# Kernel optimization log

Hardware: AMD Instinct MI355X
Metric: run time of the kernel (lower is better)

The kernel has to match this reference:

```python
import jax, jax.numpy as jnp
import numpy as np

N_NODES = 10000
N_EDGES = 80000
IN_DIM = 768
HID = 256
HEADS = 8
NEG_SLOPE = 0.2


def setup_inputs() -> dict:
    key = jax.random.key(0)
    ks = jax.random.split(key, 12)
    s = 0.02
    x = jax.random.normal(ks[0], (N_NODES, IN_DIM), dtype=jnp.float32)
    edge_index = jax.random.randint(ks[1], (2, N_EDGES), 0, N_NODES, dtype=jnp.int64)
    W1 = jax.random.normal(ks[2], (IN_DIM, HEADS * HID), dtype=jnp.float32) * s
    a_src1 = jax.random.normal(ks[3], (HEADS, HID), dtype=jnp.float32) * s
    a_dst1 = jax.random.normal(ks[4], (HEADS, HID), dtype=jnp.float32) * s
    b1 = jnp.zeros((HEADS * HID,), dtype=jnp.float32)
    W2 = jax.random.normal(ks[5], (HEADS * HID, HEADS * HID), dtype=jnp.float32) * s
    a_src2 = jax.random.normal(ks[6], (HEADS, HID), dtype=jnp.float32) * s
    a_dst2 = jax.random.normal(ks[7], (HEADS, HID), dtype=jnp.float32) * s
    b2 = jnp.zeros((HID,), dtype=jnp.float32)
    # graph_projection: 256 -> 256
    Wp = jax.random.normal(ks[8], (HID, HID), dtype=jnp.float32) * s
    bp = jnp.zeros((HID,), dtype=jnp.float32)
    return dict(x=x, edge_index=edge_index, W1=W1, a_src1=a_src1, a_dst1=a_dst1,
                b1=b1, W2=W2, a_src2=a_src2, a_dst2=a_dst2, b2=b2, Wp=Wp, bp=bp)


def _gat_conv(x, src, dst, W, a_src, a_dst, b, concat):
    """PyG GATConv (eval mode, self-loops already appended to src/dst)."""
    N = x.shape[0]
    H, C = a_src.shape
    h = (x @ W).reshape(N, H, C)                         # [N,H,C] per-head projection
    alpha_s = jnp.sum(h * a_src[None], axis=-1)           # [N,H]
    alpha_d = jnp.sum(h * a_dst[None], axis=-1)           # [N,H]
    e = jax.nn.leaky_relu(alpha_s[src] + alpha_d[dst], NEG_SLOPE)  # [E,H]
    # segment softmax over incoming edges of each dst node
    m = jax.ops.segment_max(e, dst, num_segments=N)       # [N,H]
    m = jnp.where(jnp.isfinite(m), m, 0.0)
    p = jnp.exp(e - m[dst])
    denom = jax.ops.segment_sum(p, dst, num_segments=N)   # [N,H]
    alpha = p / (denom[dst] + 1e-16)                      # [E,H]
    out = jax.ops.segment_sum(alpha[:, :, None] * h[src], dst, num_segments=N)  # [N,H,C]
    if concat:
        return out.reshape(N, H * C) + b
    return out.mean(axis=1) + b


def reference(x, edge_index, W1, a_src1, a_dst1, b1, W2, a_src2, a_dst2, b2, Wp, bp):
    N = x.shape[0]
    loops = jnp.arange(N, dtype=edge_index.dtype)
    src = jnp.concatenate([edge_index[0], loops])
    dst = jnp.concatenate([edge_index[1], loops])
    h = _gat_conv(x, src, dst, W1, a_src1, a_dst1, b1, concat=True)   # [N, 2048]
    h = jax.nn.elu(h)                                                 # dropout: eval/no-op
    h = _gat_conv(h, src, dst, W2, a_src2, a_dst2, b2, concat=False)  # [N, 256]
    h = h @ Wp + bp
    return jax.nn.relu(h)                                             # dropout: eval/no-op
```

## Files before the change

kernel.cpp:

```cpp
#include <hip/hip_runtime.h>
#include <cstdint>
#include <cstddef>

#define IN_DIM  768
#define NNODES  10000
#define MPAD    10240
#define NEDGES  80000
#define E_TOT   90000
#define HEADS   8
#define HID     256
#define HC      2048
#define NEG_SLOPE 0.2f

#define CVT_BLK  ((MPAD * IN_DIM / 4) / 256)
#define CNT_BLK  ((E_TOT + 255) / 256)
#define T1_BLK   ((HC / 32) * (IN_DIM / 32))
#define T2_BLK   ((HC / 32) * (HC / 32))
#define TP_BLK   ((HID / 32) * (HID / 32))
#define PREP_BLK (CVT_BLK + CNT_BLK + T1_BLK + T2_BLK + TP_BLK)

typedef _Float16 __attribute__((ext_vector_type(8))) f16x8;
typedef float    __attribute__((ext_vector_type(4))) f32x4;

__device__ __forceinline__ int edge_src(const int* __restrict__ ei, int e) {
    return (e < NEDGES) ? ei[e] : (e - NEDGES);
}
__device__ __forceinline__ int edge_dst(const int* __restrict__ ei, int e) {
    return (e < NEDGES) ? ei[NEDGES + e] : (e - NEDGES);
}

__device__ __forceinline__ void tcvt_body(
    const float* __restrict__ W, _Float16* __restrict__ T,
    int K, int N, int bx, int by, int t)
{
    __shared__ float tile[32][33];
    int tx = t & 31, ty = t >> 5;
#pragma unroll
    for (int q = 0; q < 4; q++)
        tile[ty + q * 8][tx] = W[(size_t)(by * 32 + ty + q * 8) * N + bx * 32 + tx];
    __syncthreads();
#pragma unroll
    for (int q = 0; q < 4; q++) {
        float v = tile[tx][ty + q * 8];
        T[(size_t)(bx * 32 + ty + q * 8) * K + by * 32 + tx] = (_Float16)v;
    }
}

__global__ __launch_bounds__(256) void prep_kernel(
    const float* __restrict__ x, _Float16* __restrict__ xh,
    const int* __restrict__ ei, int* __restrict__ cnt,
    const float* __restrict__ W1, _Float16* __restrict__ W1t,
    const float* __restrict__ W2, _Float16* __restrict__ W2t,
    const float* __restrict__ Wp, _Float16* __restrict__ Wpt)
{
    int b = blockIdx.x;
    int t = threadIdx.x;
    if (b < CVT_BLK) {
        int i = b * 256 + t;
        size_t e = (size_t)i * 4;
        int r = (int)(e / IN_DIM);
        float4 v = (r < NNODES) ? *(const float4*)(x + e)
                                : make_float4(0.f, 0.f, 0.f, 0.f);
        _Float16 h4[4] = {(_Float16)v.x, (_Float16)v.y, (_Float16)v.z, (_Float16)v.w};
        *(ushort4*)(xh + e) = *(ushort4*)h4;
    } else if (b < CVT_BLK + CNT_BLK) {
        int e = (b - CVT_BLK) * 256 + t;
        if (e < E_TOT) atomicAdd(&cnt[edge_dst(ei, e)], 1);
    } else if (b < CVT_BLK + CNT_BLK + T1_BLK) {
        int idx = b - (CVT_BLK + CNT_BLK);
        tcvt_body(W1, W1t, IN_DIM, HC, idx % (HC / 32), idx / (HC / 32), t);
    } else if (b < CVT_BLK + CNT_BLK + T1_BLK + T2_BLK) {
        int idx = b - (CVT_BLK + CNT_BLK + T1_BLK);
        tcvt_body(W2, W2t, HC, HC, idx % (HC / 32), idx / (HC / 32), t);
    } else {
        int idx = b - (CVT_BLK + CNT_BLK + T1_BLK + T2_BLK);
        tcvt_body(Wp, Wpt, HID, HID, idx % (HID / 32), idx / (HID / 32), t);
    }
}

__global__ void scan_kernel(const int* __restrict__ cnt, int* __restrict__ indptr) {
    __shared__ int sums[1024];
    const int CH = 10;
    int t = threadIdx.x;
    int base = t * CH;
    int s = 0;
#pragma unroll
    for (int i = 0; i < CH; i++) { int idx = base + i; if (idx < NNODES) s += cnt[idx]; }
    sums[t] = s;
    __syncthreads();
    for (int off = 1; off < 1024; off <<= 1) {
        int v = (t >= off) ? sums[t - off] : 0;
        __syncthreads();
        sums[t] += v;
        __syncthreads();
    }
    int run = (t == 0) ? 0 : sums[t - 1];
#pragma unroll
    for (int i = 0; i < CH; i++) {
        int idx = base + i;
        if (idx < NNODES) { indptr[idx] = run; run += cnt[idx]; }
    }
    if (t == 0) indptr[NNODES] = E_TOT;
}

__global__ void scatter_kernel(const int* __restrict__ ei, const int* __restrict__ indptr,
                               int* __restrict__ cur, int* __restrict__ sorted) {
    int e = blockIdx.x * 256 + threadIdx.x;
    if (e < E_TOT) {
        int d = edge_dst(ei, e);
        int pos = atomicAdd(&cur[d], 1);
        sorted[indptr[d] + pos] = e;
    }
}

__global__ __launch_bounds__(512, 2) void gemm8p_kernel(
    const _Float16* __restrict__ A, const _Float16* __restrict__ B,
    _Float16* __restrict__ C, int M, int K, int Nn)
{
    __shared__ __align__(16) _Float16 lds[2][36864];

    const int t = threadIdx.x;
    const int w = t >> 6, lane = t & 63;
    const int fr = lane & 15, q4 = lane >> 4;
    const int wr = w >> 2, wc = w & 3;

    const int nwgx = gridDim.x;
    int wg = blockIdx.y * nwgx + blockIdx.x;
    const int cpx = (nwgx * gridDim.y) >> 3;
    wg = (wg & 7) * cpx + (wg >> 3);
    const int row0 = (wg / nwgx) * 320;
    const int col0 = (wg % nwgx) * 256;

    const int rowt = t >> 3;
    const int scol = ((t & 7) ^ (rowt & 7)) << 3;
    const _Float16* baseA = A + (size_t)(row0 + rowt) * K + scol;
    const _Float16* baseB = B + (size_t)(col0 + rowt) * K + scol;
    const int dstw = w * 512;

    auto stageA = [&](int q, int kel, int bb) {
        __builtin_amdgcn_global_load_lds(
            (const __attribute__((address_space(1))) void*)(baseA + (size_t)q * 64 * K + kel),
            (__attribute__((address_space(3))) void*)&lds[bb][q * 4096 + dstw], 16, 0, 0);
    };
    auto stageB = [&](int q, int kel, int bb) {
        __builtin_amdgcn_global_load_lds(
            (const __attribute__((address_space(1))) void*)(baseB + (size_t)q * 64 * K + kel),
            (__attribute__((address_space(3))) void*)&lds[bb][20480 + q * 4096 + dstw], 16, 0, 0);
    };

    f32x4 acc[2][2][5][2];
#pragma unroll
    for (int qm = 0; qm < 2; qm++)
#pragma unroll
        for (int qn = 0; qn < 2; qn++)
#pragma unroll
            for (int mi = 0; mi < 5; mi++)
#pragma unroll
                for (int ni = 0; ni < 2; ni++)
                    acc[qm][qn][mi][ni] = {0.f, 0.f, 0.f, 0.f};

#define PHASE(QM, QN, BB, STAGE_STMT, WAIT_STMT)                                \
    do {                                                                        \
        f16x8 fa[5][2], fb[2][2];                                               \
        _Pragma("unroll")                                                       \
        for (int mi = 0; mi < 5; mi++) {                                        \
            _Pragma("unroll")                                                   \
            for (int ks = 0; ks < 2; ks++) {                                    \
                int lr = wr * 80 + mi * 16 + fr;                                \
                int sl = ((ks << 2) | q4) ^ (fr & 7);                           \
                fa[mi][ks] = *(const f16x8*)&lds[BB][(QM) * 10240 + (lr << 6) + (sl << 3)]; \
            }                                                                   \
        }                                                                       \
        _Pragma("unroll")                                                       \
        for (int ni = 0; ni < 2; ni++) {                                        \
            _Pragma("unroll")                                                   \
            for (int ks = 0; ks < 2; ks++) {                                    \
                int lr = wc * 32 + ni * 16 + fr;                                \
                int sl = ((ks << 2) | q4) ^ (fr & 7);                           \
                fb[ni][ks] = *(const f16x8*)&lds[BB][20480 + (QN) * 8192 + (lr << 6) + (sl << 3)]; \
            }                                                                   \
        }                                                                       \
        STAGE_STMT;                                                             \
        WAIT_STMT;                                                              \
        __builtin_amdgcn_s_barrier();                                           \
        asm volatile("s_waitcnt lgkmcnt(0)" ::: "memory");                      \
        __builtin_amdgcn_sched_barrier(0);                                      \
        __builtin_amdgcn_s_setprio(1);                                          \
        _Pragma("unroll")                                                       \
        for (int ks = 0; ks < 2; ks++) {                                        \
            _Pragma("unroll")                                                   \
            for (int mi = 0; mi < 5; mi++) {                                    \
                _Pragma("unroll")                                               \
                for (int ni = 0; ni < 2; ni++)                                  \
                    acc[QM][QN][mi][ni] = __builtin_amdgcn_mfma_f32_16x16x32_f16(\
                        fa[mi][ks], fb[ni][ks], acc[QM][QN][mi][ni], 0, 0, 0);  \
            }                                                                   \
        }                                                                       \
        __builtin_amdgcn_s_setprio(0);                                          \
        __builtin_amdgcn_sched_barrier(0);                                      \
        __builtin_amdgcn_s_barrier();                                           \
    } while (0)

#pragma unroll
    for (int q = 0; q < 5; q++) stageA(q, 0, 0);
#pragma unroll
    for (int q = 0; q < 4; q++) stageB(q, 0, 0);
    asm volatile("s_waitcnt vmcnt(0)" ::: "memory");
    __builtin_amdgcn_s_barrier();

    const int nT = K >> 6;
    int t0 = 0;
    for (; t0 < nT - 1; ++t0) {
        int bb = t0 & 1;
        int bn = bb ^ 1;
        int k1 = (t0 + 1) << 6;
        PHASE(0, 0, bb,
              { stageA(0, k1, bn); stageA(1, k1, bn); },
              asm volatile("s_waitcnt vmcnt(6)" ::: "memory"));
        PHASE(1, 0, bb,
              { stageA(2, k1, bn); stageB(0, k1, bn); stageB(1, k1, bn); },
              asm volatile("s_waitcnt vmcnt(7)" ::: "memory"));
        PHASE(0, 1, bb,
              { stageA(3, k1, bn); stageA(4, k1, bn); },
              asm volatile("s_waitcnt vmcnt(7)" ::: "memory"));
        PHASE(1, 1, bb,
              { stageB(2, k1, bn); stageB(3, k1, bn); },
              ((void)0));
    }
    {
        int bb = t0 & 1;
        PHASE(0, 0, bb, ((void)0), asm volatile("s_waitcnt vmcnt(4)" ::: "memory"));
        PHASE(1, 0, bb, ((void)0), asm volatile("s_waitcnt vmcnt(2)" ::: "memory"));
        PHASE(0, 1, bb, ((void)0), asm volatile("s_waitcnt vmcnt(0)" ::: "memory"));
        PHASE(1, 1, bb, ((void)0), ((void)0));
    }
#undef PHASE

#pragma unroll
    for (int qm = 0; qm < 2; qm++)
#pragma unroll
        for (int qn = 0; qn < 2; qn++)
#pragma unroll
            for (int mi = 0; mi < 5; mi++) {
                int mb = row0 + qm * 160 + wr * 80 + mi * 16 + q4 * 4;
#pragma unroll
                for (int ni = 0; ni < 2; ni++) {
                    int n = col0 + qn * 128 + wc * 32 + ni * 16 + fr;
#pragma unroll
                    for (int r = 0; r < 4; r++) {
                        int m = mb + r;
                        if (m < M) C[(size_t)m * Nn + n] = (_Float16)acc[qm][qn][mi][ni][r];
                    }
                }
            }
}

template <int EPI>
__global__ __launch_bounds__(256) void mfma_gemm_kernel(
    const _Float16* __restrict__ A, const _Float16* __restrict__ B,
    void* __restrict__ Cout, const float* __restrict__ bias,
    int M, int K, int Nn, int swz)
{
    __shared__ __align__(16) _Float16 sA[2][128 * 32];
    __shared__ __align__(16) _Float16 sB[2][128 * 32];

    int t = threadIdx.x;
    int bx = blockIdx.x, by = blockIdx.y;
    if (swz) {
        int id = by * 16 + bx;
        int xcd = id & 7, slot = id >> 3;
        bx = 2 * xcd + (slot & 1);
        by = slot >> 1;
    }
    int row0 = by * 128;
    int col0 = bx * 128;

    int s0 = t, s1 = t + 256;
    int m0 = s0 >> 2, k0 = (s0 & 3) * 8;
    int m1 = s1 >> 2, k1 = (s1 & 3) * 8;
    const _Float16* a0 = A + (size_t)(row0 + m0) * K + k0;
    const _Float16* a1 = A + (size_t)(row0 + m1) * K + k1;
    const _Float16* b0 = B + (size_t)(col0 + m0) * K + k0;
    const _Float16* b1 = B + (size_t)(col0 + m1) * K + k1;

    int w = t >> 6, lane = t & 63;
    int wm = (w & 1) * 64, wn = (w >> 1) * 64;
    int fr = lane & 15, quad = lane >> 4;

    auto stage = [&](int kt, int bsel) {
        _Float16* dA0 = &sA[bsel][(w * 64) * 8];
        _Float16* dA1 = &sA[bsel][(w * 64 + 256) * 8];
        _Float16* dB0 = &sB[bsel][(w * 64) * 8];
        _Float16* dB1 = &sB[bsel][(w * 64 + 256) * 8];
        __builtin_amdgcn_global_load_lds(
            (const __attribute__((address_space(1))) void*)(a0 + kt),
            (__attribute__((address_space(3))) void*)dA0, 16, 0, 0);
        __builtin_amdgcn_global_load_lds(
            (const __attribute__((address_space(1))) void*)(a1 + kt),
            (__attribute__((address_space(3))) void*)dA1, 16, 0, 0);
        __builtin_amdgcn_global_load_lds(
            (const __attribute__((address_space(1))) void*)(b0 + kt),
            (__attribute__((address_space(3))) void*)dB0, 16, 0, 0);
        __builtin_amdgcn_global_load_lds(
            (const __attribute__((address_space(1))) void*)(b1 + kt),
            (__attribute__((address_space(3))) void*)dB1, 16, 0, 0);
    };

    f32x4 acc[4][4];
#pragma unroll
    for (int i = 0; i < 4; i++)
#pragma unroll
        for (int j = 0; j < 4; j++) acc[i][j] = {0.f, 0.f, 0.f, 0.f};

    const int nIt = K / 32;
    stage(0, 0);
    __syncthreads();

    for (int it = 0; it < nIt; ++it) {
        int cb = it & 1;
        if (it + 1 < nIt) stage((it + 1) * 32, cb ^ 1);

        f16x8 fa[4], fb[4];
#pragma unroll
        for (int i = 0; i < 4; i++) {
            fa[i] = *(const f16x8*)&sA[cb][(wm + i * 16 + fr) * 32 + quad * 8];
            fb[i] = *(const f16x8*)&sB[cb][(wn + i * 16 + fr) * 32 + quad * 8];
        }
#pragma unroll
        for (int i = 0; i < 4; i++)
#pragma unroll
            for (int j = 0; j < 4; j++)
                acc[i][j] = __builtin_amdgcn_mfma_f32_16x16x32_f16(fa[i], fb[j], acc[i][j], 0, 0, 0);

        if (it + 1 < nIt) __syncthreads();
    }

    if (EPI == 0) {
        _Float16* C = (_Float16*)Cout;
#pragma unroll
        for (int i = 0; i < 4; i++) {
            int mbase = row0 + wm + i * 16 + quad * 4;
#pragma unroll
            for (int j = 0; j < 4; j++) {
                int n = col0 + wn + j * 16 + fr;
#pragma unroll
                for (int r = 0; r < 4; r++) {
                    int m = mbase + r;
                    if (m < M) C[(size_t)m * Nn + n] = (_Float16)acc[i][j][r];
                }
            }
        }
    } else {
        float* C = (float*)Cout;
        float bv[4];
#pragma unroll
        for (int j = 0; j < 4; j++) bv[j] = bias[col0 + wn + j * 16 + fr];
#pragma unroll
        for (int i = 0; i < 4; i++) {
            int mbase = row0 + wm + i * 16 + quad * 4;
#pragma unroll
            for (int j = 0; j < 4; j++) {
                int n = col0 + wn + j * 16 + fr;
#pragma unroll
                for (int r = 0; r < 4; r++) {
                    int m = mbase + r;
                    if (m < M) C[(size_t)m * Nn + n] = fmaxf(acc[i][j][r] + bv[j], 0.f);
                }
            }
        }
    }
}

__global__ __launch_bounds__(256) void attn_kernel(
    const _Float16* __restrict__ H, const float* __restrict__ a_src,
    const float* __restrict__ a_dst, float* __restrict__ as_out,
    float* __restrict__ ad_out)
{
    int n = blockIdx.x;
    int t = threadIdx.x;
    int h = t >> 5, l = t & 31;
    f16x8 hv = *(const f16x8*)&H[(size_t)n * HC + h * HID + l * 8];
    const float* asp = a_src + h * HID + l * 8;
    const float* adp = a_dst + h * HID + l * 8;
    float sa = 0.f, sd = 0.f;
#pragma unroll
    for (int q = 0; q < 8; q++) {
        float v = (float)hv[q];
        sa = fmaf(v, asp[q], sa);
        sd = fmaf(v, adp[q], sd);
    }
#pragma unroll
    for (int o = 16; o > 0; o >>= 1) {
        sa += __shfl_xor(sa, o, 32);
        sd += __shfl_xor(sd, o, 32);
    }
    if (l == 0) { as_out[n * HEADS + h] = sa; ad_out[n * HEADS + h] = sd; }
}

template <int MODE>
__global__ __launch_bounds__(256) void agg_kernel(
    const _Float16* __restrict__ H, const float* __restrict__ as_,
    const float* __restrict__ ad_, const float* __restrict__ bias,
    const int* __restrict__ indptr, const int* __restrict__ sorted,
    const int* __restrict__ ei, _Float16* __restrict__ outh)
{
    __shared__ float m8[HEADS], d8[HEADS], adl[HEADS];
    __shared__ int   srcl[64];
    __shared__ float al[64][HEADS];
    __shared__ float red[HC];

    int n = blockIdx.x;
    int t = threadIdx.x;

    if (n >= NNODES) {
        if (MODE == 0) {
            _Float16 z8[8] = {};
            *(f16x8*)&outh[(size_t)n * HC + t * 8] = *(f16x8*)z8;
        } else {
            outh[(size_t)n * HID + t] = (_Float16)0.f;
        }
        return;
    }

    int start = indptr[n];
    int deg = indptr[n + 1] - start;

    if (t < HEADS) adl[t] = ad_[n * HEADS + t];
    __syncthreads();

    int h = t >> 5, l = t & 31;
    float adh = adl[h];

    float mx = -1e30f;
    for (int j = l; j < deg; j += 32) {
        int e = sorted[start + j];
        int s = edge_src(ei, e);
        float v = as_[s * HEADS + h] + adh;
        v = (v >= 0.f) ? v : NEG_SLOPE * v;
        mx = fmaxf(mx, v);
    }
#pragma unroll
    for (int o = 16; o > 0; o >>= 1) mx = fmaxf(mx, __shfl_xor(mx, o, 32));

    float sm = 0.f;
    for (int j = l; j < deg; j += 32) {
        int e = sorted[start + j];
        int s = edge_src(ei, e);
        float v = as_[s * HEADS + h] + adh;
        v = (v >= 0.f) ? v : NEG_SLOPE * v;
        sm += expf(v - mx);
    }
#pragma unroll
    for (int o = 16; o > 0; o >>= 1) sm += __shfl_xor(sm, o, 32);
    if (l == 0) { m8[h] = mx; d8[h] = sm; }

    int hh = t >> 5, c8 = (t & 31) * 8;
    const size_t hoff = (size_t)hh * HID + c8;
    float acc[8] = {};
    for (int base = 0; base < deg; base += 64) {
        int cntc = min(64, deg - base);
        __syncthreads();
        if (t < cntc) srcl[t] = edge_src(ei, sorted[start + base + t]);
        __syncthreads();
        {
            int j = t & 63, h0 = t >> 6;
            if (j < cntc) {
#pragma unroll
                for (int q = 0; q < 2; q++) {
                    int hx = h0 + q * 4;
                    float v = as_[srcl[j] * HEADS + hx] + adl[hx];
                    v = (v >= 0.f) ? v : NEG_SLOPE * v;
                    al[j][hx] = expf(v - m8[hx]) / (d8[hx] + 1e-16f);
                }
            }
        }
        __syncthreads();
        int jj = 0;
        for (; jj + 3 < cntc; jj += 4) {
            int sx0 = srcl[jj + 0], sx1 = srcl[jj + 1];
            int sx2 = srcl[jj + 2], sx3 = srcl[jj + 3];
            f16x8 h0v = *(const f16x8*)&H[(size_t)sx0 * HC + hoff];
            f16x8 h1v = *(const f16x8*)&H[(size_t)sx1 * HC + hoff];
            f16x8 h2v = *(const f16x8*)&H[(size_t)sx2 * HC + hoff];
            f16x8 h3v = *(const f16x8*)&H[(size_t)sx3 * HC + hoff];
            float a0 = al[jj + 0][hh], a1 = al[jj + 1][hh];
            float a2 = al[jj + 2][hh], a3 = al[jj + 3][hh];
#pragma unroll
            for (int q = 0; q < 8; q++) acc[q] = fmaf(a0, (float)h0v[q], acc[q]);
#pragma unroll
            for (int q = 0; q < 8; q++) acc[q] = fmaf(a1, (float)h1v[q], acc[q]);
#pragma unroll
            for (int q = 0; q < 8; q++) acc[q] = fmaf(a2, (float)h2v[q], acc[q]);
#pragma unroll
            for (int q = 0; q < 8; q++) acc[q] = fmaf(a3, (float)h3v[q], acc[q]);
        }
        for (; jj < cntc; jj++) {
            int s = srcl[jj];
            f16x8 hv = *(const f16x8*)&H[(size_t)s * HC + hoff];
            float a = al[jj][hh];
#pragma unroll
            for (int q = 0; q < 8; q++)
                acc[q] = fmaf(a, (float)hv[q], acc[q]);
        }
    }

    if (MODE == 0) {
        _Float16 o8[8];
#pragma unroll
        for (int q = 0; q < 8; q++) {
            float v = acc[q] + bias[hoff + q];
            v = (v > 0.f) ? v : expm1f(v);
            o8[q] = (_Float16)v;
        }
        *(f16x8*)&outh[(size_t)n * HC + hoff] = *(f16x8*)o8;
    } else {
#pragma unroll
        for (int q = 0; q < 8; q++) red[hoff + q] = acc[q];
        __syncthreads();
        float s = 0.f;
#pragma unroll
        for (int h2 = 0; h2 < HEADS; h2++) s += red[h2 * HID + t];
        outh[(size_t)n * HID + t] = (_Float16)(s * 0.125f + bias[t]);
    }
}

extern "C" void kernel_launch(void* const* d_in, const int* in_sizes, int n_in,
                              void* d_out, int out_size, void* d_ws, size_t ws_size,
                              hipStream_t stream)
{
    const float* x      = (const float*)d_in[0];
    const int*   ei     = (const int*)  d_in[1];
    const float* W1     = (const float*)d_in[2];
    const float* a_src1 = (const float*)d_in[3];
    const float* a_dst1 = (const float*)d_in[4];
    const float* b1     = (const float*)d_in[5];
    const float* W2     = (const float*)d_in[6];
    const float* a_src2 = (const float*)d_in[7];
    const float* a_dst2 = (const float*)d_in[8];
    const float* b2     = (const float*)d_in[9];
    const float* Wp     = (const float*)d_in[10];
    const float* bp     = (const float*)d_in[11];
    float* out = (float*)d_out;

    char* ws = (char*)d_ws;
    size_t off = 0;
    auto alloc = [&](size_t bytes) -> char* {
        char* p = ws + off;
        off += (bytes + 255) & ~(size_t)255;
        return p;
    };
    _Float16* Hbuf = (_Float16*)alloc((size_t)NNODES * HC * 2);
    _Float16* A2   = (_Float16*)alloc((size_t)MPAD * HC * 2);
    _Float16* W1t  = (_Float16*)alloc((size_t)HC * IN_DIM * 2);
    _Float16* W2t  = (_Float16*)alloc((size_t)HC * HC * 2);
    _Float16* Wpt  = (_Float16*)alloc((size_t)HID * HID * 2);
    _Float16* xh   = (_Float16*)alloc((size_t)MPAD * IN_DIM * 2);
    _Float16* out2h = (_Float16*)alloc((size_t)MPAD * HID * 2);
    float* asad   = (float*)alloc((size_t)4 * NNODES * HEADS * sizeof(float));
    float* as1 = asad;
    float* ad1 = asad + (size_t)NNODES * HEADS;
    float* as2 = asad + (size_t)2 * NNODES * HEADS;
    float* ad2 = asad + (size_t)3 * NNODES * HEADS;
    int*   cntcur = (int*)alloc((size_t)2 * NNODES * sizeof(int));
    int*   cnt = cntcur;
    int*   cur = cntcur + NNODES;
    int*   indptr = (int*)  alloc((size_t)(NNODES + 1) * sizeof(int));
    int*   sorted = (int*)  alloc((size_t)E_TOT * sizeof(int));

    hipMemsetAsync(cntcur, 0, (size_t)2 * NNODES * sizeof(int), stream);
    prep_kernel<<<PREP_BLK, 256, 0, stream>>>(x, xh, ei, cnt,
                                              W1, W1t, W2, W2t, Wp, Wpt);
    scan_kernel<<<1, 1024, 0, stream>>>(cnt, indptr);
    scatter_kernel<<<(E_TOT + 255) / 256, 256, 0, stream>>>(ei, indptr, cur, sorted);

    dim3 g8(HC / 256, MPAD / 320);

    gemm8p_kernel<<<g8, 512, 0, stream>>>(xh, W1t, Hbuf, NNODES, IN_DIM, HC);
    attn_kernel<<<NNODES, 256, 0, stream>>>(Hbuf, a_src1, a_dst1, as1, ad1);
    agg_kernel<0><<<MPAD, 256, 0, stream>>>(Hbuf, as1, ad1, b1, indptr, sorted, ei, A2);

    gemm8p_kernel<<<g8, 512, 0, stream>>>(A2, W2t, Hbuf, NNODES, HC, HC);
    attn_kernel<<<NNODES, 256, 0, stream>>>(Hbuf, a_src2, a_dst2, as2, ad2);
    agg_kernel<1><<<MPAD, 256, 0, stream>>>(Hbuf, as2, ad2, b2, indptr, sorted, ei, out2h);

    dim3 gProj(HID / 128, MPAD / 128);
    mfma_gemm_kernel<1><<<gProj, 256, 0, stream>>>(out2h, Wpt, out, bp,
                                                   NNODES, HID, HID, 0);
}
```

Baseline: 413.0 us.

## Reorder GEMM quadrant phases to reuse LDS fragments and drop trailing barrier

The 2x2 quadrant phases of the fp16 MFMA GEMM loop are reordered in a serpentine pattern (00, 01, 11, 10), so each phase reloads only the A or the B fragment that changed and reuses the other from registers. This cuts LDS reads per K-tile. The trailing barrier in each phase is removed and the vmcnt waits and global-to-LDS staging order are rebalanced, which cuts synchronisation. The risk is a subtle LDS race: loads of the next buffer could overwrite data still being read, and fragments now stay live longer, which raises register pressure.

New measurement: 406.3 us. No clear change (-1.6%).

```diff
diff --git a/kernel.cpp b/kernel.cpp
--- a/kernel.cpp
+++ b/kernel.cpp
@@ -159,9 +159,10 @@
                 for (int ni = 0; ni < 2; ni++)
                     acc[qm][qn][mi][ni] = {0.f, 0.f, 0.f, 0.f};
 
-#define PHASE(QM, QN, BB, STAGE_STMT, WAIT_STMT)                                \
-    do {                                                                        \
-        f16x8 fa[5][2], fb[2][2];                                               \
+    f16x8 fa[5][2], fb[2][2];
+
+#define LOADA(BB, QM)                                                           \
+    {                                                                           \
         _Pragma("unroll")                                                       \
         for (int mi = 0; mi < 5; mi++) {                                        \
             _Pragma("unroll")                                                   \
@@ -171,6 +172,9 @@
                 fa[mi][ks] = *(const f16x8*)&lds[BB][(QM) * 10240 + (lr << 6) + (sl << 3)]; \
             }                                                                   \
         }                                                                       \
+    }
+#define LOADB(BB, QN)                                                           \
+    {                                                                           \
         _Pragma("unroll")                                                       \
         for (int ni = 0; ni < 2; ni++) {                                        \
             _Pragma("unroll")                                                   \
@@ -180,9 +184,14 @@
                 fb[ni][ks] = *(const f16x8*)&lds[BB][20480 + (QN) * 8192 + (lr << 6) + (sl << 3)]; \
             }                                                                   \
         }                                                                       \
-        STAGE_STMT;                                                             \
+    }
+
+#define PHASE(QM, QN, LOAD_STMT, STAGE_STMT, WAIT_STMT)                         \
+    do {                                                                        \
         WAIT_STMT;                                                              \
         __builtin_amdgcn_s_barrier();                                           \
+        LOAD_STMT;                                                              \
+        STAGE_STMT;                                                             \
         asm volatile("s_waitcnt lgkmcnt(0)" ::: "memory");                      \
         __builtin_amdgcn_sched_barrier(0);                                      \
         __builtin_amdgcn_s_setprio(1);                                          \
@@ -198,15 +207,14 @@
         }                                                                       \
         __builtin_amdgcn_s_setprio(0);                                          \
         __builtin_amdgcn_sched_barrier(0);                                      \
-        __builtin_amdgcn_s_barrier();                                           \
     } while (0)
 
-#pragma unroll
-    for (int q = 0; q < 5; q++) stageA(q, 0, 0);
-#pragma unroll
-    for (int q = 0; q < 4; q++) stageB(q, 0, 0);
-    asm volatile("s_waitcnt vmcnt(0)" ::: "memory");
-    __builtin_amdgcn_s_barrier();
+#define VM(N) asm volatile("s_waitcnt vmcnt(" #N ")" ::: "memory")
+
+    stageA(0, 0, 0); stageA(1, 0, 0); stageA(2, 0, 0);
+    stageB(0, 0, 0); stageB(1, 0, 0);
+    stageB(2, 0, 0); stageB(3, 0, 0);
+    stageA(3, 0, 0); stageA(4, 0, 0);
 
     const int nT = K >> 6;
     int t0 = 0;
@@ -214,27 +222,30 @@
         int bb = t0 & 1;
         int bn = bb ^ 1;
         int k1 = (t0 + 1) << 6;
-        PHASE(0, 0, bb,
-              { stageA(0, k1, bn); stageA(1, k1, bn); },
-              asm volatile("s_waitcnt vmcnt(6)" ::: "memory"));
-        PHASE(1, 0, bb,
-              { stageA(2, k1, bn); stageB(0, k1, bn); stageB(1, k1, bn); },
-              asm volatile("s_waitcnt vmcnt(7)" ::: "memory"));
-        PHASE(0, 1, bb,
+        PHASE(0, 0, { LOADA(bb, 0); LOADB(bb, 0); },
+              { stageA(0, k1, bn); stageA(1, k1, bn); stageA(2, k1, bn); },
+              VM(4));
+        PHASE(0, 1, { LOADB(bb, 1); },
+              { stageB(0, k1, bn); stageB(1, k1, bn); },
+              VM(5));
+        PHASE(1, 1, { LOADA(bb, 1); },
+              { stageB(2, k1, bn); stageB(3, k1, bn); },
+              VM(5));
+        PHASE(1, 0, { LOADB(bb, 0); },
               { stageA(3, k1, bn); stageA(4, k1, bn); },
-              asm volatile("s_waitcnt vmcnt(7)" ::: "memory"));
-        PHASE(1, 1, bb,
-              { stageB(2, k1, bn); stageB(3, k1, bn); },
               ((void)0));
     }
     {
         int bb = t0 & 1;
-        PHASE(0, 0, bb, ((void)0), asm volatile("s_waitcnt vmcnt(4)" ::: "memory"));
-        PHASE(1, 0, bb, ((void)0), asm volatile("s_waitcnt vmcnt(2)" ::: "memory"));
-        PHASE(0, 1, bb, ((void)0), asm volatile("s_waitcnt vmcnt(0)" ::: "memory"));
-        PHASE(1, 1, bb, ((void)0), ((void)0));
+        PHASE(0, 0, { LOADA(bb, 0); LOADB(bb, 0); }, ((void)0), VM(4));
+        PHASE(0, 1, { LOADB(bb, 1); },               ((void)0), VM(2));
+        PHASE(1, 1, { LOADA(bb, 1); },               ((void)0), VM(0));
+        PHASE(1, 0, { LOADB(bb, 0); },               ((void)0), ((void)0));
     }
 #undef PHASE
+#undef LOADA
+#undef LOADB
+#undef VM
 
 #pragma unroll
     for (int qm = 0; qm < 2; qm++)
```
